# Optimization experiments

Hardware: AMD Instinct MI355X
Metric: run time of the kernel (lower is better)

Reference implementation:

```python
import jax, jax.numpy as jnp
import numpy as np

CHANNELS = 256

def setup_inputs() -> dict:
    key = jax.random.key(0)
    ks = jax.random.split(key, 7)
    B, C, N = 4, CHANNELS, 4096
    scale = 1.0 / np.sqrt(C)
    x = jax.random.normal(ks[0], (B, C, N), dtype=jnp.float32)
    Wq = jax.random.normal(ks[1], (C, C), dtype=jnp.float32) * scale
    bq = jax.random.normal(ks[2], (C,), dtype=jnp.float32) * 0.01
    Wk = jax.random.normal(ks[3], (C, C), dtype=jnp.float32) * scale
    bk = jax.random.normal(ks[4], (C,), dtype=jnp.float32) * 0.01
    Wv = jax.random.normal(ks[5], (C, C), dtype=jnp.float32) * scale
    bv = jax.random.normal(ks[6], (C,), dtype=jnp.float32) * 0.01
    return {"x": x, "Wq": Wq, "bq": bq, "Wk": Wk, "bk": bk, "Wv": Wv, "bv": bv}

def reference(x, Wq, bq, Wk, bk, Wv, bv):
    # x: [B, C, N]; 1x1 Conv1d == channel-mixing matmul
    C = x.shape[1]
    Q = jnp.einsum('oc,bcn->bon', Wq, x) + bq[None, :, None]   # [B, C, N]
    K = jnp.einsum('oc,bcn->bon', Wk, x) + bk[None, :, None]   # [B, C, N]
    V = jnp.einsum('oc,bcn->bon', Wv, x) + bv[None, :, None]   # [B, C, N]
    # attn[b, i, j] = softmax_j( Q[:, i]^T K[:, j] / sqrt(C) )
    scores = jnp.einsum('bci,bcj->bij', Q, K) / jnp.sqrt(jnp.asarray(C, x.dtype))
    attn = jax.nn.softmax(scores, axis=-1)                     # [B, N, N]
    context = jnp.einsum('bij,bcj->bci', attn, V)              # [B, C, N]
    return x + context
```

## Files before the change

kernel.cpp:

```cpp
#include <hip/hip_runtime.h>
#include <stdint.h>

#define B_ 4
#define C_ 256
#define N_ 4096
#define JS 4

typedef unsigned short u16;
typedef __attribute__((ext_vector_type(4))) float f32x4;
typedef __attribute__((ext_vector_type(16))) float f32x16;
typedef __attribute__((ext_vector_type(8))) short bf16x8;
typedef __attribute__((ext_vector_type(4))) int i32x4;

__device__ __forceinline__ u16 f2bf(float f) {
    uint32_t u = __float_as_uint(f);
    u += 0x7fffu + ((u >> 16) & 1u);
    return (u16)(u >> 16);
}
__device__ __forceinline__ float bf2f(u16 v) {
    uint32_t u = ((uint32_t)v) << 16;
    return __uint_as_float(u);
}
__device__ __forceinline__ uint32_t pkbf(float a, float b) {
    uint32_t ua = __float_as_uint(a) + 0x8000u;
    uint32_t ub = __float_as_uint(b) + 0x8000u;
    return (ua >> 16) | (ub & 0xffff0000u);
}

#if defined(__has_builtin)
#if __has_builtin(__builtin_amdgcn_global_load_lds)
#define HAVE_GLL 1
#endif
#endif

#ifdef HAVE_GLL
__device__ __forceinline__ void g2l16(const u16* g, u16* lbase, int lane) {
    (void)lane;
    __builtin_amdgcn_global_load_lds(
        (__attribute__((address_space(1))) void*)(uintptr_t)g,
        (__attribute__((address_space(3))) void*)lbase, 16, 0, 0);
}
#else
__device__ __forceinline__ void g2l16(const u16* g, u16* lbase, int lane) {
    *(i32x4*)(lbase + lane * 8) = *(const i32x4*)g;
}
#endif

__global__ __launch_bounds__(256) void wconv_kernel(
    const float* __restrict__ Wq, const float* __restrict__ Wk,
    const float* __restrict__ Wv, u16* __restrict__ Wb) {
    int id = blockIdx.x * 256 + threadIdx.x;
    const float* src = (id < 65536) ? Wq : ((id < 131072) ? Wk : Wv);
    Wb[id] = f2bf(src[id & 65535]);
}

#define OSS 264
#define VSS 40
__global__ __launch_bounds__(256, 2) void qkv_kernel(
    const float* __restrict__ x, const u16* __restrict__ Wb,
    const float* __restrict__ bq, const float* __restrict__ bk,
    const float* __restrict__ bv,
    u16* __restrict__ Qt, u16* __restrict__ Kt, u16* __restrict__ Vt) {
    __shared__ __align__(16) u16 smem[256 * VSS];

    int blk = blockIdx.x;
    int n0  = (blk & 127) << 5;
    int b   = blk >> 7;
    int tid = threadIdx.x;
    int lane = tid & 63;
    int w = tid >> 6;
    int l31 = lane & 31;
    int h = lane >> 5;

    {
        int c0 = tid >> 3;
        int nq = (tid & 7) << 2;
        const float* xb = x + ((size_t)b * C_ + c0) * N_ + n0 + nq;
        #pragma unroll
        for (int p = 0; p < 8; ++p) {
            f32x4 v = *(const f32x4*)(xb + (size_t)32 * N_ * p);
            int cc = c0 + 32 * p;
            smem[(nq + 0) * OSS + cc] = f2bf(v[0]);
            smem[(nq + 1) * OSS + cc] = f2bf(v[1]);
            smem[(nq + 2) * OSS + cc] = f2bf(v[2]);
            smem[(nq + 3) * OSS + cc] = f2bf(v[3]);
        }
    }
    __syncthreads();

    bf16x8 xf[16];
    #pragma unroll
    for (int ks = 0; ks < 16; ++ks)
        xf[ks] = *(const bf16x8*)(&smem[l31 * OSS + 16 * ks + 8 * h]);
    __syncthreads();

    #pragma unroll
    for (int mat = 0; mat < 2; ++mat) {
        const u16* W = Wb + mat * 65536;
        const float* bias = mat ? bk : bq;
        u16* dst = mat ? Kt : Qt;
        f32x16 acc0, acc1;
        #pragma unroll
        for (int r = 0; r < 16; ++r) { acc0[r] = 0.f; acc1[r] = 0.f; }
        const u16* wr0 = W + (size_t)(64 * w + l31) * 256 + 8 * h;
        const u16* wr1 = W + (size_t)(64 * w + 32 + l31) * 256 + 8 * h;
        #pragma unroll
        for (int ks = 0; ks < 16; ++ks) {
            bf16x8 wf0 = *(const bf16x8*)(wr0 + 16 * ks);
            bf16x8 wf1 = *(const bf16x8*)(wr1 + 16 * ks);
            acc0 = __builtin_amdgcn_mfma_f32_32x32x16_bf16(xf[ks], wf0, acc0, 0, 0, 0);
            acc1 = __builtin_amdgcn_mfma_f32_32x32x16_bf16(xf[ks], wf1, acc1, 0, 0, 0);
        }
        #pragma unroll
        for (int ot = 0; ot < 2; ++ot) {
            const f32x16& a = ot ? acc1 : acc0;
            int c = 64 * w + 32 * ot + l31;
            float bo = bias[c];
            #pragma unroll
            for (int g = 0; g < 4; ++g)
                #pragma unroll
                for (int r = 0; r < 4; ++r)
                    smem[(8 * g + 4 * h + r) * OSS + c] = f2bf(a[4 * g + r] + bo);
        }
        __syncthreads();
        #pragma unroll
        for (int p = 0; p < 4; ++p) {
            int row = 8 * p + (tid >> 5);
            int chunk = tid & 31;
            int cswz = mat ? (chunk ^ row) : chunk;
            i32x4 v = *(const i32x4*)(smem + row * OSS + chunk * 8);
            *(i32x4*)(dst + ((size_t)b * N_ + n0 + row) * C_ + cswz * 8) = v;
        }
        __syncthreads();
    }

    {
        const u16* W = Wb + 2 * 65536;
        f32x16 acc0, acc1;
        #pragma unroll
        for (int r = 0; r < 16; ++r) { acc0[r] = 0.f; acc1[r] = 0.f; }
        const u16* wr0 = W + (size_t)(64 * w + l31) * 256 + 8 * h;
        const u16* wr1 = W + (size_t)(64 * w + 32 + l31) * 256 + 8 * h;
        #pragma unroll
        for (int ks = 0; ks < 16; ++ks) {
            bf16x8 wf0 = *(const bf16x8*)(wr0 + 16 * ks);
            bf16x8 wf1 = *(const bf16x8*)(wr1 + 16 * ks);
            acc0 = __builtin_amdgcn_mfma_f32_32x32x16_bf16(wf0, xf[ks], acc0, 0, 0, 0);
            acc1 = __builtin_amdgcn_mfma_f32_32x32x16_bf16(wf1, xf[ks], acc1, 0, 0, 0);
        }
        #pragma unroll
        for (int mt = 0; mt < 2; ++mt) {
            const f32x16& a = mt ? acc1 : acc0;
            #pragma unroll
            for (int g = 0; g < 4; ++g)
                #pragma unroll
                for (int r = 0; r < 4; ++r) {
                    int o = 64 * w + 32 * mt + 8 * g + 4 * h + r;
                    smem[o * VSS + l31] = f2bf(a[4 * g + r] + bv[o]);
                }
        }
        __syncthreads();
        int tb = n0 & ~63;
        int hb = (n0 & 32) >> 3;
        #pragma unroll
        for (int p = 0; p < 4; ++p) {
            int o = 64 * p + (tid >> 2);
            int chunk = tid & 3;
            int cswz = (hb + chunk) ^ (o & 7);
            i32x4 v = *(const i32x4*)(smem + o * VSS + chunk * 8);
            *(i32x4*)(Vt + ((size_t)b * C_ + o) * N_ + tb + cswz * 8) = v;
        }
    }
}

__device__ __forceinline__ void stage64(const u16* Kb, const u16* Vb, int j0,
                                        u16* ksd, u16* vsd, int w, int lane) {
    const u16* kg = Kb + (size_t)(j0 + 16 * w) * C_ + lane * 8;
    u16* kdb = ksd + 16 * w * 256;
    #pragma unroll
    for (int rr = 0; rr < 8; ++rr)
        g2l16(kg + rr * 512, kdb + rr * 512, lane);
    const u16* vg = Vb + (size_t)(64 * w + (lane >> 3)) * N_ + j0 + (lane & 7) * 8;
    u16* vdb = vsd + 64 * w * 64;
    #pragma unroll
    for (int rr = 0; rr < 8; ++rr)
        g2l16(vg + (size_t)8 * rr * N_, vdb + rr * 512, lane);
}

__global__ __launch_bounds__(256, 2) void attn_kernel(
    const u16* __restrict__ Qt, const u16* __restrict__ Kt,
    const u16* __restrict__ Vt, u16* __restrict__ Op,
    float* __restrict__ lArr) {
    __shared__ __align__(16) u16 Ksh[64 * 256];
    __shared__ __align__(16) u16 Vsh[256 * 64];

    int blk = blockIdx.x;
    int it = blk & 31;
    int b  = (blk >> 5) & 3;
    int s  = blk >> 7;
    int i0 = it << 7;
    int tid = threadIdx.x;
    int lane = tid & 63;
    int w = tid >> 6;
    int l31 = lane & 31;
    int h = lane >> 5;

    bf16x8 qf[16];
    {
        const u16* qrow = Qt + ((size_t)b * N_ + i0 + 32 * w + l31) * C_ + 8 * h;
        #pragma unroll
        for (int ks = 0; ks < 16; ++ks) qf[ks] = *(const bf16x8*)(qrow + 16 * ks);
    }

    f32x16 oacc[8];
    #pragma unroll
    for (int mt = 0; mt < 8; ++mt)
        #pragma unroll
        for (int r = 0; r < 16; ++r) oacc[mt][r] = 0.f;
    float l_run = 0.f;

    const float sconst = 0.0625f * 1.44269504088896340736f;
    const u16* Kb = Kt + (size_t)b * N_ * C_;
    const u16* Vb = Vt + (size_t)b * C_ * N_;
    int jbase = s * (N_ / JS);
    const int T = N_ / (64 * JS);

    stage64(Kb, Vb, jbase, Ksh, Vsh, w, lane);
    __syncthreads();

    for (int jt = 0; jt < T; ++jt) {
        f32x16 st0, st1;
        #pragma unroll
        for (int r = 0; r < 16; ++r) { st0[r] = 0.f; st1[r] = 0.f; }
        #pragma unroll
        for (int ks = 0; ks < 16; ++ks) {
            int kc = ((2 * ks + h) ^ l31) << 3;
            bf16x8 kf0 = *(const bf16x8*)(Ksh + l31 * 256 + kc);
            bf16x8 kf1 = *(const bf16x8*)(Ksh + (32 + l31) * 256 + kc);
            st0 = __builtin_amdgcn_mfma_f32_32x32x16_bf16(kf0, qf[ks], st0, 0, 0, 0);
            st1 = __builtin_amdgcn_mfma_f32_32x32x16_bf16(kf1, qf[ks], st1, 0, 0, 0);
        }

        float psum = 0.f;
        uint32_t pd[16];
        #pragma unroll
        for (int u = 0; u < 8; ++u) {
            const f32x16& stv = (u < 4) ? st0 : st1;
            int g = u & 3;
            #pragma unroll
            for (int d = 0; d < 2; ++d) {
                float p0 = exp2f(stv[4 * g + 2 * d + 0] * sconst);
                float p1 = exp2f(stv[4 * g + 2 * d + 1] * sconst);
                psum += p0 + p1;
                pd[u * 2 + d] = pkbf(p0, p1);
            }
        }
        psum += __shfl_xor(psum, 32);
        l_run += psum;

        bf16x8 pf[4];
        #pragma unroll
        for (int ks2 = 0; ks2 < 4; ++ks2) {
            uint32_t oA0 = pd[4 * ks2 + 0], oA1 = pd[4 * ks2 + 1];
            uint32_t oB0 = pd[4 * ks2 + 2], oB1 = pd[4 * ks2 + 3];
            uint32_t sn0 = h ? oA0 : oB0, sn1 = h ? oA1 : oB1;
            uint32_t rc0 = (uint32_t)__shfl_xor((int)sn0, 32);
            uint32_t rc1 = (uint32_t)__shfl_xor((int)sn1, 32);
            uint32_t ow0 = h ? oB0 : oA0, ow1 = h ? oB1 : oA1;
            i32x4 fr;
            fr[0] = (int)(h ? rc0 : ow0);
            fr[1] = (int)(h ? rc1 : ow1);
            fr[2] = (int)(h ? ow0 : rc0);
            fr[3] = (int)(h ? ow1 : rc1);
            pf[ks2] = *(bf16x8*)&fr;
        }

        #pragma unroll
        for (int ks2 = 0; ks2 < 4; ++ks2) {
            int vc = ((2 * ks2 + h) ^ (l31 & 7)) << 3;
            #pragma unroll
            for (int mt = 0; mt < 8; ++mt) {
                bf16x8 vf = *(const bf16x8*)(Vsh + (32 * mt + l31) * 64 + vc);
                oacc[mt] = __builtin_amdgcn_mfma_f32_32x32x16_bf16(vf, pf[ks2], oacc[mt], 0, 0, 0);
            }
        }

        if (jt + 1 < T) {
            __syncthreads();
            stage64(Kb, Vb, jbase + (jt + 1) * 64, Ksh, Vsh, w, lane);
            __syncthreads();
        }
    }

    int i = i0 + 32 * w + l31;
    u16* ob = Op + ((size_t)(s * B_ + b) * C_) * N_ + i;
    #pragma unroll
    for (int mt = 0; mt < 8; ++mt)
        #pragma unroll
        for (int g = 0; g < 4; ++g)
            #pragma unroll
            for (int r = 0; r < 4; ++r) {
                int c = 32 * mt + 8 * g + r + 4 * h;
                ob[(size_t)c * N_] = f2bf(oacc[mt][4 * g + r]);
            }
    if (h == 0) lArr[(size_t)(s * B_ + b) * N_ + i] = l_run;
}

__global__ __launch_bounds__(256) void merge_kernel(
    const float* __restrict__ x, const u16* __restrict__ Op,
    const float* __restrict__ lArr, float* __restrict__ out) {
    int blk = blockIdx.x;
    int b  = blk >> 7;
    int i4 = (blk & 127) * 32 + (threadIdx.x & 7) * 4;
    int cb = threadIdx.x >> 3;

    f32x4 L = {0.f, 0.f, 0.f, 0.f};
    #pragma unroll
    for (int s = 0; s < JS; ++s) {
        f32x4 lv = *(const f32x4*)(lArr + (size_t)(s * B_ + b) * N_ + i4);
        L += lv;
    }
    f32x4 rL;
    #pragma unroll
    for (int k = 0; k < 4; ++k) rL[k] = 1.0f / L[k];

    #pragma unroll
    for (int kk = 0; kk < 8; ++kk) {
        int c = kk * 32 + cb;
        size_t xi = ((size_t)b * C_ + c) * N_ + i4;
        f32x4 acc = {0.f, 0.f, 0.f, 0.f};
        #pragma unroll
        for (int s = 0; s < JS; ++s) {
            const u16* op = Op + ((size_t)(s * B_ + b) * C_ + c) * N_ + i4;
            ushort2 v01 = *(const ushort2*)(op);
            ushort2 v23 = *(const ushort2*)(op + 2);
            acc[0] += bf2f(v01.x);
            acc[1] += bf2f(v01.y);
            acc[2] += bf2f(v23.x);
            acc[3] += bf2f(v23.y);
        }
        f32x4 xv = *(const f32x4*)(x + xi);
        f32x4 ov;
        #pragma unroll
        for (int k = 0; k < 4; ++k) ov[k] = fmaf(acc[k], rL[k], xv[k]);
        *(f32x4*)(out + xi) = ov;
    }
}

extern "C" void kernel_launch(void* const* d_in, const int* in_sizes, int n_in,
                              void* d_out, int out_size, void* d_ws, size_t ws_size,
                              hipStream_t stream) {
    const float* x  = (const float*)d_in[0];
    const float* Wq = (const float*)d_in[1];
    const float* bq = (const float*)d_in[2];
    const float* Wk = (const float*)d_in[3];
    const float* bk = (const float*)d_in[4];
    const float* Wv = (const float*)d_in[5];
    const float* bv = (const float*)d_in[6];
    float* out = (float*)d_out;

    u16* Wb = (u16*)d_ws;
    u16* Qt = Wb + 3 * 65536;
    u16* Kt = Qt + (size_t)B_ * N_ * C_;
    u16* Vt = Kt + (size_t)B_ * N_ * C_;
    u16* Op = Vt + (size_t)B_ * N_ * C_;
    float* lArr = (float*)(Op + (size_t)JS * B_ * C_ * N_);

    wconv_kernel<<<768, 256, 0, stream>>>(Wq, Wk, Wv, Wb);
    qkv_kernel<<<512, 256, 0, stream>>>(x, Wb, bq, bk, bv, Qt, Kt, Vt);
    attn_kernel<<<512, 256, 0, stream>>>(Qt, Kt, Vt, Op, lArr);
    merge_kernel<<<512, 256, 0, stream>>>(x, Op, lArr, out);
}
```

Measured before the change: 204.0 us.

## Use FP8 for V and probabilities in the attention PV matmul

Stores V as FP8 (e4m3) from the QKV projection and packs the softmax probabilities to FP8. The P·V product then runs on the 32x32x16 fp8 MFMA instead of bf16. This halves V's global and LDS traffic and simplifies the cross-half lane shuffle for the P fragments. It trades accuracy, since FP8 has coarse mantissa and limited range for unnormalized exp values, and the merge kernel's loads are also widened to ushort4.

```diff
diff --git a/kernel.cpp b/kernel.cpp
--- a/kernel.cpp
+++ b/kernel.cpp
@@ -7,6 +7,8 @@
 #define JS 4
 
 typedef unsigned short u16;
+typedef unsigned char u8;
+typedef long i64;
 typedef __attribute__((ext_vector_type(4))) float f32x4;
 typedef __attribute__((ext_vector_type(16))) float f32x16;
 typedef __attribute__((ext_vector_type(8))) short bf16x8;
@@ -21,11 +23,37 @@
     uint32_t u = ((uint32_t)v) << 16;
     return __uint_as_float(u);
 }
-__device__ __forceinline__ uint32_t pkbf(float a, float b) {
-    uint32_t ua = __float_as_uint(a) + 0x8000u;
-    uint32_t ub = __float_as_uint(b) + 0x8000u;
-    return (ua >> 16) | (ub & 0xffff0000u);
-}
+
+#if defined(__has_builtin)
+#if __has_builtin(__builtin_amdgcn_cvt_pk_fp8_f32)
+#define HAVE_CVTFP8 1
+#endif
+#endif
+
+#ifdef HAVE_CVTFP8
+template <bool HI>
+__device__ __forceinline__ uint32_t pk2fp8(float a, float b, uint32_t old) {
+    return (uint32_t)__builtin_amdgcn_cvt_pk_fp8_f32(a, b, (int)old, HI);
+}
+#else
+__device__ __forceinline__ uint32_t fp8_1(float x) {
+    uint32_t u = __float_as_uint(x);
+    uint32_t s = (u >> 24) & 0x80u;
+    float ax = fabsf(x);
+    if (ax < 0.0078125f) return s;
+    if (ax > 448.f) return s | 0x7eu;
+    uint32_t m = u & 0x7fffffffu;
+    m += 0x7ffffu + ((m >> 20) & 1u);
+    int e = (int)(m >> 23) - 127;
+    if (e < -6) return s;
+    return s | ((uint32_t)(e + 7) << 3) | ((m >> 20) & 7u);
+}
+template <bool HI>
+__device__ __forceinline__ uint32_t pk2fp8(float a, float b, uint32_t old) {
+    uint32_t lo = fp8_1(a) | (fp8_1(b) << 8);
+    return HI ? ((old & 0xffffu) | (lo << 16)) : ((old & 0xffff0000u) | lo);
+}
+#endif
 
 #if defined(__has_builtin)
 #if __has_builtin(__builtin_amdgcn_global_load_lds)
@@ -60,7 +88,7 @@
     const float* __restrict__ x, const u16* __restrict__ Wb,
     const float* __restrict__ bq, const float* __restrict__ bk,
     const float* __restrict__ bv,
-    u16* __restrict__ Qt, u16* __restrict__ Kt, u16* __restrict__ Vt) {
+    u16* __restrict__ Qt, u16* __restrict__ Kt, u8* __restrict__ Vt8) {
     __shared__ __align__(16) u16 smem[256 * VSS];
 
     int blk = blockIdx.x;
@@ -167,32 +195,37 @@
             int o = 64 * p + (tid >> 2);
             int chunk = tid & 3;
             int cswz = (hb + chunk) ^ (o & 7);
-            i32x4 v = *(const i32x4*)(smem + o * VSS + chunk * 8);
-            *(i32x4*)(Vt + ((size_t)b * C_ + o) * N_ + tb + cswz * 8) = v;
-        }
-    }
-}
-
-__device__ __forceinline__ void stage64(const u16* Kb, const u16* Vb, int j0,
-                                        u16* ksd, u16* vsd, int w, int lane) {
+            const u16* vs = smem + o * VSS + chunk * 8;
+            float f0 = bf2f(vs[0]), f1 = bf2f(vs[1]), f2 = bf2f(vs[2]), f3 = bf2f(vs[3]);
+            float f4 = bf2f(vs[4]), f5 = bf2f(vs[5]), f6 = bf2f(vs[6]), f7 = bf2f(vs[7]);
+            uint32_t d0 = pk2fp8<false>(f0, f1, 0); d0 = pk2fp8<true>(f2, f3, d0);
+            uint32_t d1 = pk2fp8<false>(f4, f5, 0); d1 = pk2fp8<true>(f6, f7, d1);
+            uint2 st = {d0, d1};
+            *(uint2*)(Vt8 + ((size_t)b * C_ + o) * N_ + tb + cswz * 8) = st;
+        }
+    }
+}
+
+__device__ __forceinline__ void stage64(const u16* Kb, const u8* Vb8, int j0,
+                                        u16* ksd, u8* vsd, int w, int lane) {
     const u16* kg = Kb + (size_t)(j0 + 16 * w) * C_ + lane * 8;
     u16* kdb = ksd + 16 * w * 256;
     #pragma unroll
     for (int rr = 0; rr < 8; ++rr)
         g2l16(kg + rr * 512, kdb + rr * 512, lane);
-    const u16* vg = Vb + (size_t)(64 * w + (lane >> 3)) * N_ + j0 + (lane & 7) * 8;
-    u16* vdb = vsd + 64 * w * 64;
-    #pragma unroll
-    for (int rr = 0; rr < 8; ++rr)
-        g2l16(vg + (size_t)8 * rr * N_, vdb + rr * 512, lane);
+    const u8* vg = Vb8 + (size_t)(64 * w + (lane >> 2)) * N_ + j0 + (lane & 3) * 16;
+    u8* vdb = vsd + 64 * w * 64;
+    #pragma unroll
+    for (int rr = 0; rr < 4; ++rr)
+        g2l16((const u16*)(vg + (size_t)16 * rr * N_), (u16*)(vdb + rr * 1024), lane);
 }
 
 __global__ __launch_bounds__(256, 2) void attn_kernel(
     const u16* __restrict__ Qt, const u16* __restrict__ Kt,
-    const u16* __restrict__ Vt, u16* __restrict__ Op,
+    const u8* __restrict__ Vt8, u16* __restrict__ Op,
     float* __restrict__ lArr) {
     __shared__ __align__(16) u16 Ksh[64 * 256];
-    __shared__ __align__(16) u16 Vsh[256 * 64];
+    __shared__ __align__(16) u8 Vsh8[256 * 64];
 
     int blk = blockIdx.x;
     int it = blk & 31;
@@ -221,11 +254,11 @@
 
     const float sconst = 0.0625f * 1.44269504088896340736f;
     const u16* Kb = Kt + (size_t)b * N_ * C_;
-    const u16* Vb = Vt + (size_t)b * C_ * N_;
+    const u8* Vb8 = Vt8 + (size_t)b * C_ * N_;
     int jbase = s * (N_ / JS);
     const int T = N_ / (64 * JS);
 
-    stage64(Kb, Vb, jbase, Ksh, Vsh, w, lane);
+    stage64(Kb, Vb8, jbase, Ksh, Vsh8, w, lane);
     __syncthreads();
 
     for (int jt = 0; jt < T; ++jt) {
@@ -242,52 +275,41 @@
         }
 
         float psum = 0.f;
-        uint32_t pd[16];
+        uint32_t pd[8];
         #pragma unroll
         for (int u = 0; u < 8; ++u) {
             const f32x16& stv = (u < 4) ? st0 : st1;
             int g = u & 3;
-            #pragma unroll
-            for (int d = 0; d < 2; ++d) {
-                float p0 = exp2f(stv[4 * g + 2 * d + 0] * sconst);
-                float p1 = exp2f(stv[4 * g + 2 * d + 1] * sconst);
-                psum += p0 + p1;
-                pd[u * 2 + d] = pkbf(p0, p1);
-            }
+            float p0 = exp2f(stv[4 * g + 0] * sconst);
+            float p1 = exp2f(stv[4 * g + 1] * sconst);
+            float p2 = exp2f(stv[4 * g + 2] * sconst);
+            float p3 = exp2f(stv[4 * g + 3] * sconst);
+            psum += (p0 + p1) + (p2 + p3);
+            uint32_t t = pk2fp8<false>(p0, p1, 0);
+            pd[u] = pk2fp8<true>(p2, p3, t);
         }
         psum += __shfl_xor(psum, 32);
         l_run += psum;
 
-        bf16x8 pf[4];
         #pragma unroll
         for (int ks2 = 0; ks2 < 4; ++ks2) {
-            uint32_t oA0 = pd[4 * ks2 + 0], oA1 = pd[4 * ks2 + 1];
-            uint32_t oB0 = pd[4 * ks2 + 2], oB1 = pd[4 * ks2 + 3];
-            uint32_t sn0 = h ? oA0 : oB0, sn1 = h ? oA1 : oB1;
-            uint32_t rc0 = (uint32_t)__shfl_xor((int)sn0, 32);
-            uint32_t rc1 = (uint32_t)__shfl_xor((int)sn1, 32);
-            uint32_t ow0 = h ? oB0 : oA0, ow1 = h ? oB1 : oA1;
-            i32x4 fr;
-            fr[0] = (int)(h ? rc0 : ow0);
-            fr[1] = (int)(h ? rc1 : ow1);
-            fr[2] = (int)(h ? ow0 : rc0);
-            fr[3] = (int)(h ? ow1 : rc1);
-            pf[ks2] = *(bf16x8*)&fr;
-        }
-
-        #pragma unroll
-        for (int ks2 = 0; ks2 < 4; ++ks2) {
+            int qo = 2 * ks2 + h;
+            int qs = 2 * ks2 + 1 - h;
+            uint32_t recv = (uint32_t)__shfl_xor((int)pd[qs], 32);
+            uint32_t d0 = h ? recv : pd[qo];
+            uint32_t d1 = h ? pd[qo] : recv;
+            i64 pb = (i64)(((uint64_t)d1 << 32) | (uint64_t)d0);
             int vc = ((2 * ks2 + h) ^ (l31 & 7)) << 3;
             #pragma unroll
             for (int mt = 0; mt < 8; ++mt) {
-                bf16x8 vf = *(const bf16x8*)(Vsh + (32 * mt + l31) * 64 + vc);
-                oacc[mt] = __builtin_amdgcn_mfma_f32_32x32x16_bf16(vf, pf[ks2], oacc[mt], 0, 0, 0);
+                i64 vv = *(const i64*)(Vsh8 + (32 * mt + l31) * 64 + vc);
+                oacc[mt] = __builtin_amdgcn_mfma_f32_32x32x16_fp8_fp8(vv, pb, oacc[mt], 0, 0, 0);
             }
         }
 
         if (jt + 1 < T) {
             __syncthreads();
-            stage64(Kb, Vb, jbase + (jt + 1) * 64, Ksh, Vsh, w, lane);
+            stage64(Kb, Vb8, jbase + (jt + 1) * 64, Ksh, Vsh8, w, lane);
             __syncthreads();
         }
     }
@@ -331,13 +353,11 @@
         f32x4 acc = {0.f, 0.f, 0.f, 0.f};
         #pragma unroll
         for (int s = 0; s < JS; ++s) {
-            const u16* op = Op + ((size_t)(s * B_ + b) * C_ + c) * N_ + i4;
-            ushort2 v01 = *(const ushort2*)(op);
-            ushort2 v23 = *(const ushort2*)(op + 2);
-            acc[0] += bf2f(v01.x);
-            acc[1] += bf2f(v01.y);
-            acc[2] += bf2f(v23.x);
-            acc[3] += bf2f(v23.y);
+            ushort4 v = *(const ushort4*)(Op + ((size_t)(s * B_ + b) * C_ + c) * N_ + i4);
+            acc[0] += bf2f(v.x);
+            acc[1] += bf2f(v.y);
+            acc[2] += bf2f(v.z);
+            acc[3] += bf2f(v.w);
         }
         f32x4 xv = *(const f32x4*)(x + xi);
         f32x4 ov;
@@ -362,12 +382,12 @@
     u16* Wb = (u16*)d_ws;
     u16* Qt = Wb + 3 * 65536;
     u16* Kt = Qt + (size_t)B_ * N_ * C_;
-    u16* Vt = Kt + (size_t)B_ * N_ * C_;
-    u16* Op = Vt + (size_t)B_ * N_ * C_;
+    u8*  Vt8 = (u8*)(Kt + (size_t)B_ * N_ * C_);
+    u16* Op = (u16*)(Vt8 + (size_t)B_ * C_ * N_);
     float* lArr = (float*)(Op + (size_t)JS * B_ * C_ * N_);
 
     wconv_kernel<<<768, 256, 0, stream>>>(Wq, Wk, Wv, Wb);
-    qkv_kernel<<<512, 256, 0, stream>>>(x, Wb, bq, bk, bv, Qt, Kt, Vt);
-    attn_kernel<<<512, 256, 0, stream>>>(Qt, Kt, Vt, Op, lArr);
+    qkv_kernel<<<512, 256, 0, stream>>>(x, Wb, bq, bk, bv, Qt, Kt, Vt8);
+    attn_kernel<<<512, 256, 0, stream>>>(Qt, Kt, Vt8, Op, lArr);
     merge_kernel<<<512, 256, 0, stream>>>(x, Op, lArr, out);
 }
```

Result: slower. 209.8 us (+2.8%).
